# Optimization experiments

Hardware: AMD Instinct MI355X
Metric: run time of the kernel (lower is better)

## Reference

```python
import jax, jax.numpy as jnp
import numpy as np

B, C, H, W = 1, 320, 64, 64
HEADS, DHEAD = 8, 40
INNER = HEADS * DHEAD          # 320 == C (as in Stable Diffusion)
CTX_LEN, CTX_DIM = 77, 768
FF_INNER = 4 * INNER           # 1280
GROUPS, GN_EPS, LN_EPS = 32, 1e-6, 1e-5
SCALE = DHEAD ** -0.5


def setup_inputs() -> dict:
    key = jax.random.key(0)
    ks = jax.random.split(key, 16)
    def w(k, shape):
        return jax.random.normal(k, shape, jnp.float32) * 0.02
    return {
        'x': jax.random.normal(ks[0], (B, C, H, W), jnp.float32),
        'context': jax.random.normal(ks[1], (B, CTX_LEN, CTX_DIM), jnp.float32),
        'gn_scale': jnp.ones((C,), jnp.float32),
        'gn_bias': jnp.zeros((C,), jnp.float32),
        'w_proj_in': w(ks[2], (C, INNER)), 'b_proj_in': jnp.zeros((INNER,), jnp.float32),
        'ln1_s': jnp.ones((INNER,), jnp.float32), 'ln1_b': jnp.zeros((INNER,), jnp.float32),
        'wq1': w(ks[3], (INNER, INNER)), 'wk1': w(ks[4], (INNER, INNER)),
        'wv1': w(ks[5], (INNER, INNER)), 'wo1': w(ks[6], (INNER, INNER)),
        'bo1': jnp.zeros((INNER,), jnp.float32),
        'ln2_s': jnp.ones((INNER,), jnp.float32), 'ln2_b': jnp.zeros((INNER,), jnp.float32),
        'wq2': w(ks[7], (INNER, INNER)), 'wk2': w(ks[8], (CTX_DIM, INNER)),
        'wv2': w(ks[9], (CTX_DIM, INNER)), 'wo2': w(ks[10], (INNER, INNER)),
        'bo2': jnp.zeros((INNER,), jnp.float32),
        'ln3_s': jnp.ones((INNER,), jnp.float32), 'ln3_b': jnp.zeros((INNER,), jnp.float32),
        'w_ff1': w(ks[11], (INNER, 2 * FF_INNER)), 'b_ff1': jnp.zeros((2 * FF_INNER,), jnp.float32),
        'w_ff2': w(ks[12], (FF_INNER, INNER)), 'b_ff2': jnp.zeros((INNER,), jnp.float32),
        'w_proj_out': w(ks[13], (INNER, C)), 'b_proj_out': jnp.zeros((C,), jnp.float32),
    }


def _group_norm(x, scale, bias):
    b, c, h, w = x.shape
    xg = x.reshape(b, GROUPS, c // GROUPS, h, w)
    mu = xg.mean(axis=(2, 3, 4), keepdims=True)
    var = xg.var(axis=(2, 3, 4), keepdims=True)
    xg = (xg - mu) * jax.lax.rsqrt(var + GN_EPS)
    return xg.reshape(b, c, h, w) * scale[None, :, None, None] + bias[None, :, None, None]


def _layer_norm(x, s, b):
    mu = x.mean(-1, keepdims=True)
    var = x.var(-1, keepdims=True)
    return (x - mu) * jax.lax.rsqrt(var + LN_EPS) * s + b


def _attention(xq, ctx, wq, wk, wv, wo, bo):
    b, s, _ = xq.shape
    t = ctx.shape[1]
    q = (xq @ wq).reshape(b, s, HEADS, DHEAD)
    k = (ctx @ wk).reshape(b, t, HEADS, DHEAD)
    v = (ctx @ wv).reshape(b, t, HEADS, DHEAD)
    scores = jnp.einsum('bihd,bjhd->bhij', q, k) * SCALE  # [b,h,s,t]
    probs = jax.nn.softmax(scores, axis=-1)
    o = jnp.einsum('bhij,bjhd->bihd', probs, v).reshape(b, s, INNER)
    return o @ wo + bo


def _forward(x, context, gn_scale, gn_bias, w_proj_in, b_proj_in,
             ln1_s, ln1_b, wq1, wk1, wv1, wo1, bo1,
             ln2_s, ln2_b, wq2, wk2, wv2, wo2, bo2,
             ln3_s, ln3_b, w_ff1, b_ff1, w_ff2, b_ff2,
             w_proj_out, b_proj_out):
    x_in = x
    h_ = _group_norm(x, gn_scale, gn_bias)
    # 1x1 conv proj_in as channel matmul
    h_ = jnp.einsum('bchw,cd->bdhw', h_, w_proj_in) + b_proj_in[None, :, None, None]
    h_ = h_.transpose(0, 2, 3, 1).reshape(B, H * W, INNER)  # [b, s, d]
    # self-attention
    hn = _layer_norm(h_, ln1_s, ln1_b)
    h_ = _attention(hn, hn, wq1, wk1, wv1, wo1, bo1) + h_
    # cross-attention
    hn = _layer_norm(h_, ln2_s, ln2_b)
    h_ = _attention(hn, context, wq2, wk2, wv2, wo2, bo2) + h_
    # GEGLU feed-forward
    hn = _layer_norm(h_, ln3_s, ln3_b)
    y = hn @ w_ff1 + b_ff1
    a, g = jnp.split(y, 2, axis=-1)
    y = (a * jax.nn.gelu(g, approximate=False)) @ w_ff2 + b_ff2
    h_ = y + h_
    h_ = h_.reshape(B, H, W, INNER).transpose(0, 3, 1, 2)
    out = jnp.einsum('bchw,cd->bdhw', h_, w_proj_out) + b_proj_out[None, :, None, None]
    return out + x_in


def reference(x, context, gn_scale, gn_bias, w_proj_in, b_proj_in,
              ln1_s, ln1_b, wq1, wk1, wv1, wo1, bo1,
              ln2_s, ln2_b, wq2, wk2, wv2, wo2, bo2,
              ln3_s, ln3_b, w_ff1, b_ff1, w_ff2, b_ff2,
              w_proj_out, b_proj_out):
    return _forward(x, context, gn_scale, gn_bias, w_proj_in, b_proj_in,
                    ln1_s, ln1_b, wq1, wk1, wv1, wo1, bo1,
                    ln2_s, ln2_b, wq2, wk2, wv2, wo2, bo2,
                    ln3_s, ln3_b, w_ff1, b_ff1, w_ff2, b_ff2,
                    w_proj_out, b_proj_out)
```

## Files before the change

### kernel.cpp

```cpp
#include <hip/hip_runtime.h>
#include <hip/hip_bf16.h>
#include <math.h>

#define SCALE_L2E  0.22811011265722836f

typedef __attribute__((ext_vector_type(8))) short short8v;
typedef __attribute__((ext_vector_type(4))) float float4v;
typedef unsigned short u16;

__device__ __forceinline__ unsigned pack2(float a, float b) {
  float2 f; f.x = a; f.y = b;
  __hip_bfloat162 h = __float22bfloat162_rn(f);
  return *(unsigned*)&h;
}
__device__ __forceinline__ float bfu2f(u16 u) {
  return __uint_as_float(((unsigned)u) << 16);
}
__device__ __forceinline__ u16 f2bf(float x) {
  __hip_bfloat16 h = __float2bfloat16(x);
  return *(u16*)&h;
}

struct TDesc { const float* src; u16* dst; int K, N, off, tx; float sc; };
struct TPack { TDesc d[12]; };

__global__ __launch_bounds__(256) void prep_kernel(
    TPack p, int nT,
    const float* __restrict__ ctxsrc, u16* __restrict__ ctxdst,
    const float* __restrict__ x,
    float* __restrict__ psum, float* __restrict__ psq) {
  __shared__ float ls[32][33];
  int bt = blockIdx.x, t = threadIdx.x;
  if (bt < nT) {
    int ti = 0;
    #pragma unroll
    for (int i = 1; i < 12; i++) if (bt >= p.d[i].off) ti = i;
    TDesc dd = p.d[ti];
    int local = bt - dd.off;
    int n0 = (local % dd.tx) * 32, k0 = (local / dd.tx) * 32;
    #pragma unroll
    for (int i = 0; i < 4; i++) {
      int idx = t + i*256, r = idx >> 5, c = idx & 31;
      ls[r][c] = dd.src[(size_t)(k0 + r)*dd.N + n0 + c];
    }
    __syncthreads();
    #pragma unroll
    for (int i = 0; i < 2; i++) {
      int p2 = t + i*256, n = p2 >> 4, kp = (p2 & 15)*2;
      *(unsigned*)&dd.dst[(size_t)(n0 + n)*dd.K + k0 + kp] =
        pack2(ls[kp][n]*dd.sc, ls[kp+1][n]*dd.sc);
    }
  } else if (bt < nT + 58) {
    int idx = ((bt - nT)*256 + t)*4;
    if (idx < 59136) {
      float4 v = *(const float4*)&ctxsrc[idx];
      uint2 o; o.x = pack2(v.x, v.y); o.y = pack2(v.z, v.w);
      *(uint2*)&ctxdst[idx] = o;
    }
  } else {
    int pp = bt - nT - 58;
    int g = pp >> 3, part = pp & 7;
    size_t base = (size_t)g*40960 + (size_t)part*5120;
    float sum = 0.f, sq = 0.f;
    #pragma unroll
    for (int r = 0; r < 5; r++) {
      float4 v = *(const float4*)&x[base + (size_t)(t + r*256)*4];
      sum += v.x + v.y + v.z + v.w;
      sq  += v.x*v.x + v.y*v.y + v.z*v.z + v.w*v.w;
    }
    float* s1 = &ls[0][0];
    float* s2 = &ls[8][0] + 8;
    s1[t] = sum; s2[t] = sq; __syncthreads();
    for (int st = 128; st > 0; st >>= 1) {
      if (t < st) { s1[t] += s1[t+st]; s2[t] += s2[t+st]; }
      __syncthreads();
    }
    if (t == 0) { psum[pp] = s1[0]; psq[pp] = s2[0]; }
  }
}

__global__ __launch_bounds__(256) void gn_apply_t_kernel(
    const float* __restrict__ x, const float* __restrict__ psum,
    const float* __restrict__ psq, const float* __restrict__ gs,
    const float* __restrict__ gb, u16* __restrict__ gnT) {
  __shared__ float ts[64][65];
  __shared__ float scl[64], sft[64];
  int s0 = blockIdx.x * 64, c0 = blockIdx.y * 64;
  int t = threadIdx.x;
  if (t < 64) {
    int c = c0 + t, g = c / 10;
    float s = 0.f, q = 0.f;
    #pragma unroll
    for (int i = 0; i < 8; i++) { s += psum[g*8 + i]; q += psq[g*8 + i]; }
    float mu = s * (1.f/40960.f);
    float var = q * (1.f/40960.f) - mu*mu;
    float rs = rsqrtf(var + 1e-6f);
    float sc = rs * gs[c];
    scl[t] = sc;
    sft[t] = gb[c] - mu * sc;
  }
  int crow = t >> 2, sch = (t & 3) * 16;
  #pragma unroll
  for (int j = 0; j < 4; j++) {
    float4 v = *(const float4*)&x[(size_t)(c0 + crow)*4096 + s0 + sch + 4*j];
    ts[crow][sch + 4*j + 0] = v.x; ts[crow][sch + 4*j + 1] = v.y;
    ts[crow][sch + 4*j + 2] = v.z; ts[crow][sch + 4*j + 3] = v.w;
  }
  __syncthreads();
  int srow = t >> 2, cch = (t & 3) * 16;
  #pragma unroll
  for (int p = 0; p < 8; p++) {
    int cl = cch + 2*p;
    float f0 = ts[cl][srow] * scl[cl] + sft[cl];
    float f1 = ts[cl+1][srow] * scl[cl+1] + sft[cl+1];
    *(unsigned*)&gnT[(size_t)(s0 + srow)*320 + c0 + cl] = pack2(f0, f1);
  }
}

__global__ __launch_bounds__(64) void layernorm_kernel(
    const u16* __restrict__ X, const float* __restrict__ s,
    const float* __restrict__ b, u16* __restrict__ Y) {
  int row = blockIdx.x, t = threadIdx.x;
  const u16* xr = X + (size_t)row*320;
  float v[5], sum = 0.f, sq = 0.f;
  #pragma unroll
  for (int i = 0; i < 5; i++) { v[i] = bfu2f(xr[t + 64*i]); sum += v[i]; sq += v[i]*v[i]; }
  #pragma unroll
  for (int o = 32; o > 0; o >>= 1) { sum += __shfl_down(sum, o); sq += __shfl_down(sq, o); }
  sum = __shfl(sum, 0); sq = __shfl(sq, 0);
  float mu = sum * (1.f/320.f);
  float var = sq * (1.f/320.f) - mu*mu;
  float rs = rsqrtf(var + 1e-5f);
  u16* yr = Y + (size_t)row*320;
  #pragma unroll
  for (int i = 0; i < 5; i++) {
    int c = t + 64*i;
    yr[c] = f2bf((v[i]-mu)*rs*s[c] + b[c]);
  }
}

template<int MODE>
__global__ __launch_bounds__(256) void oneshot(
    const u16* __restrict__ A, const u16* __restrict__ BT,
    const float* __restrict__ bias, const u16* __restrict__ res,
    const float* __restrict__ xres, void* __restrict__ Cout,
    int K, int chunks) {
  __shared__ __align__(16) u16 As[64*328];
  __shared__ __align__(16) u16 Bs[32*328];
  const int t = threadIdx.x;
  const int lane = t & 63, w = t >> 6, l16 = lane & 15, g = lane >> 4;
  const int bm = blockIdx.x * 64, bn = blockIdx.y * 32;
  const int m0 = (w & 1) * 32, n0 = (w >> 1) * 16;
  float4v acc[2] = {};

  const u16* Ab = A + (size_t)(bm + (t>>2))*K + (t&3)*16;
  u16* Al = As + (t>>2)*328 + (t&3)*16;
  const u16* Bb = BT + (size_t)(bn + (t>>3))*K + (t&7)*16;
  u16* Bl = Bs + (t>>3)*328 + (t&7)*16;
  const bool b3 = (t & 7) < 4;

  for (int ch = 0; ch < chunks; ch++) {
    const int c0 = ch*320;
    __syncthreads();
    #pragma unroll
    for (int j = 0; j < 5; j++) {
      *(short8v*)(Al + 64*j)     = *(const short8v*)(Ab + c0 + 64*j);
      *(short8v*)(Al + 64*j + 8) = *(const short8v*)(Ab + c0 + 64*j + 8);
    }
    *(short8v*)Bl         = *(const short8v*)(Bb + c0);
    *(short8v*)(Bl + 8)   = *(const short8v*)(Bb + c0 + 8);
    *(short8v*)(Bl + 128) = *(const short8v*)(Bb + c0 + 128);
    *(short8v*)(Bl + 136) = *(const short8v*)(Bb + c0 + 136);
    if (b3) {
      *(short8v*)(Bl + 256) = *(const short8v*)(Bb + c0 + 256);
      *(short8v*)(Bl + 264) = *(const short8v*)(Bb + c0 + 264);
    }
    __syncthreads();
    #pragma unroll
    for (int ks = 0; ks < 10; ks++) {
      short8v bfv = *(const short8v*)&Bs[(n0 + l16)*328 + ks*32 + g*8];
      #pragma unroll
      for (int mt = 0; mt < 2; mt++) {
        short8v af = *(const short8v*)&As[(m0 + 16*mt + l16)*328 + ks*32 + g*8];
        acc[mt] = __builtin_amdgcn_mfma_f32_16x16x32_bf16(af, bfv, acc[mt], 0, 0, 0);
      }
    }
  }
  __syncthreads();
  float* Cs = (float*)As;
  #pragma unroll
  for (int mt = 0; mt < 2; mt++)
    #pragma unroll
    for (int r = 0; r < 4; r++)
      Cs[(m0 + 16*mt + 4*g + r)*36 + n0 + l16] = acc[mt][r];
  __syncthreads();

  if (MODE == 0) {
    u16* C = (u16*)Cout;
    #pragma unroll
    for (int i = 0; i < 4; i++) {
      int p = t + i*256;
      int mm = p >> 4, pp = (p & 15)*2;
      float f0 = Cs[mm*36 + pp], f1 = Cs[mm*36 + pp + 1];
      if (bias) { f0 += bias[bn + pp]; f1 += bias[bn + pp + 1]; }
      if (res) {
        unsigned u = *(const unsigned*)&res[(size_t)(bm + mm)*320 + bn + pp];
        f0 += bfu2f((u16)(u & 0xffffu));
        f1 += bfu2f((u16)(u >> 16));
      }
      *(unsigned*)&C[(size_t)(bm + mm)*320 + bn + pp] = pack2(f0, f1);
    }
  } else {
    float* C = (float*)Cout;
    int nloc = t >> 3, mch = (t & 7) * 8;
    float bb = bias[bn + nloc];
    #pragma unroll
    for (int j = 0; j < 2; j++) {
      int m4 = mch + j*4;
      float4 xv = *(const float4*)&xres[(size_t)(bn + nloc)*4096 + bm + m4];
      float4 ov;
      ov.x = Cs[(m4+0)*36 + nloc] + bb + xv.x;
      ov.y = Cs[(m4+1)*36 + nloc] + bb + xv.y;
      ov.z = Cs[(m4+2)*36 + nloc] + bb + xv.z;
      ov.w = Cs[(m4+3)*36 + nloc] + bb + xv.w;
      *(float4*)&C[(size_t)(bn + nloc)*4096 + bm + m4] = ov;
    }
  }
}

template<int MODE>
__global__ __launch_bounds__(256) void mgemm(
    const u16* __restrict__ A, const u16* __restrict__ BT,
    const float* __restrict__ bias, const u16* __restrict__ res,
    const float* __restrict__ xres, void* __restrict__ Cout,
    int M, int N, int K, int segStride) {
  __shared__ __align__(16) u16 smem[2*64*72];
  u16* As = smem;
  u16* Bs = smem + 64*72;
  const int t = threadIdx.x;
  const int lane = t & 63, w = t >> 6, l16 = lane & 15, g = lane >> 4;
  const int bm = blockIdx.x * 64, bn = blockIdx.y * 64;
  const int m0 = (w & 1) * 32, n0 = (w >> 1) * 32;
  float4v acc[2][2] = {};
  const int ar = t >> 2, ac = (t & 3) * 16;
  const bool aok = (bm + ar) < M;
  const u16* ga = &A[(size_t)(bm + ar)*K + ac];
  const u16* gb = &BT[(size_t)(bn + ar)*K + ac];

  short8v pa0 = {}, pa1 = {}, pb0, pb1;
  if (aok) { pa0 = *(const short8v*)ga; pa1 = *(const short8v*)(ga + 8); }
  pb0 = *(const short8v*)gb; pb1 = *(const short8v*)(gb + 8);

  for (int k0 = 0; k0 < K; k0 += 64) {
    __syncthreads();
    *(short8v*)&As[ar*72 + ac] = pa0;
    *(short8v*)&As[ar*72 + ac + 8] = pa1;
    *(short8v*)&Bs[ar*72 + ac] = pb0;
    *(short8v*)&Bs[ar*72 + ac + 8] = pb1;
    __syncthreads();
    if (k0 + 64 < K) {
      const u16* na = ga + k0 + 64;
      const u16* nb = gb + k0 + 64;
      if (aok) { pa0 = *(const short8v*)na; pa1 = *(const short8v*)(na + 8); }
      pb0 = *(const short8v*)nb; pb1 = *(const short8v*)(nb + 8);
    }
    #pragma unroll
    for (int ks = 0; ks < 2; ks++) {
      short8v af[2], bfv[2];
      #pragma unroll
      for (int mt = 0; mt < 2; mt++)
        af[mt] = *(const short8v*)&As[(m0 + 16*mt + l16)*72 + ks*32 + g*8];
      #pragma unroll
      for (int nt = 0; nt < 2; nt++)
        bfv[nt] = *(const short8v*)&Bs[(n0 + 16*nt + l16)*72 + ks*32 + g*8];
      #pragma unroll
      for (int mt = 0; mt < 2; mt++)
        #pragma unroll
        for (int nt = 0; nt < 2; nt++)
          acc[mt][nt] = __builtin_amdgcn_mfma_f32_16x16x32_bf16(af[mt], bfv[nt], acc[mt][nt], 0, 0, 0);
    }
  }
  __syncthreads();
  float* Cs = (float*)smem;
  #pragma unroll
  for (int mt = 0; mt < 2; mt++)
    #pragma unroll
    for (int nt = 0; nt < 2; nt++)
      #pragma unroll
      for (int r = 0; r < 4; r++)
        Cs[(m0 + 16*mt + 4*g + r)*68 + n0 + 16*nt + l16] = acc[mt][nt][r];
  __syncthreads();

  if (MODE == 1) {
    u16* C = (u16*)Cout + (size_t)(bn / 320) * segStride;
    int nb = bn % 320;
    #pragma unroll
    for (int i = 0; i < 8; i++) {
      int p = t + i*256;
      int mm = p >> 5, nn = (p & 31)*2;
      int gm = bm + mm;
      if (gm >= M) continue;
      *(unsigned*)&C[(size_t)gm*320 + nb + nn] = pack2(Cs[mm*68 + nn], Cs[mm*68 + nn + 1]);
    }
  } else if (MODE == 3) {
    if (bn < 640) {
      u16* C = (u16*)Cout + (size_t)(bn / 320) * segStride;
      int nb = bn % 320;
      #pragma unroll
      for (int i = 0; i < 8; i++) {
        int p = t + i*256;
        int mm = p >> 5, nn = (p & 31)*2;
        *(unsigned*)&C[(size_t)(bm + mm)*320 + nb + nn] = pack2(Cs[mm*68 + nn], Cs[mm*68 + nn + 1]);
      }
    } else {
      u16* vTp = (u16*)(void*)xres;
      int nloc = t >> 2, mch = (t & 3) * 16;
      int vd = bn - 640 + nloc;
      u16* dst = vTp + (size_t)vd*4096 + bm + mch;
      unsigned buf[8];
      #pragma unroll
      for (int jj = 0; jj < 8; jj++)
        buf[jj] = pack2(Cs[(mch + 2*jj)*68 + nloc], Cs[(mch + 2*jj + 1)*68 + nloc]);
      uint4 o0; o0.x = buf[0]; o0.y = buf[1]; o0.z = buf[2]; o0.w = buf[3];
      uint4 o1; o1.x = buf[4]; o1.y = buf[5]; o1.z = buf[6]; o1.w = buf[7];
      *(uint4*)dst = o0;
      *(uint4*)(dst + 8) = o1;
    }
  }
}

__global__ __launch_bounds__(256) void geglu_mfma(
    const u16* __restrict__ A, const u16* __restrict__ BT,
    const float* __restrict__ bias, u16* __restrict__ C) {
  __shared__ __align__(16) u16 smem[3*64*72];
  u16* As = smem;
  u16* Ba = smem + 64*72;
  u16* Bg = smem + 2*64*72;
  const int t = threadIdx.x;
  const int lane = t & 63, w = t >> 6, l16 = lane & 15, g = lane >> 4;
  const int bm = blockIdx.x * 64, bn = blockIdx.y * 64;
  const int m0 = (w & 1) * 32, n0 = (w >> 1) * 32;
  float4v aacc[2][2] = {}, gacc[2][2] = {};
  const int ar = t >> 2, ac = (t & 3) * 16;
  const u16* ga  = &A[(size_t)(bm + ar)*320 + ac];
  const u16* gba = &BT[(size_t)(bn + ar)*320 + ac];
  const u16* gbg = &BT[(size_t)(1280 + bn + ar)*320 + ac];

  short8v pa0 = *(const short8v*)ga,  pa1 = *(const short8v*)(ga + 8);
  short8v pb0 = *(const short8v*)gba, pb1 = *(const short8v*)(gba + 8);
  short8v pg0 = *(const short8v*)gbg, pg1 = *(const short8v*)(gbg + 8);

  for (int k0 = 0; k0 < 320; k0 += 64) {
    __syncthreads();
    *(short8v*)&As[ar*72 + ac] = pa0;
    *(short8v*)&As[ar*72 + ac + 8] = pa1;
    *(short8v*)&Ba[ar*72 + ac] = pb0;
    *(short8v*)&Ba[ar*72 + ac + 8] = pb1;
    *(short8v*)&Bg[ar*72 + ac] = pg0;
    *(short8v*)&Bg[ar*72 + ac + 8] = pg1;
    __syncthreads();
    if (k0 + 64 < 320) {
      pa0 = *(const short8v*)(ga + k0 + 64);  pa1 = *(const short8v*)(ga + k0 + 72);
      pb0 = *(const short8v*)(gba + k0 + 64); pb1 = *(const short8v*)(gba + k0 + 72);
      pg0 = *(const short8v*)(gbg + k0 + 64); pg1 = *(const short8v*)(gbg + k0 + 72);
    }
    #pragma unroll
    for (int ks = 0; ks < 2; ks++) {
      short8v af[2], bav[2], bgv[2];
      #pragma unroll
      for (int mt = 0; mt < 2; mt++)
        af[mt] = *(const short8v*)&As[(m0 + 16*mt + l16)*72 + ks*32 + g*8];
      #pragma unroll
      for (int nt = 0; nt < 2; nt++) {
        bav[nt] = *(const short8v*)&Ba[(n0 + 16*nt + l16)*72 + ks*32 + g*8];
        bgv[nt] = *(const short8v*)&Bg[(n0 + 16*nt + l16)*72 + ks*32 + g*8];
      }
      #pragma unroll
      for (int mt = 0; mt < 2; mt++)
        #pragma unroll
        for (int nt = 0; nt < 2; nt++) {
          aacc[mt][nt] = __builtin_amdgcn_mfma_f32_16x16x32_bf16(af[mt], bav[nt], aacc[mt][nt], 0, 0, 0);
          gacc[mt][nt] = __builtin_amdgcn_mfma_f32_16x16x32_bf16(af[mt], bgv[nt], gacc[mt][nt], 0, 0, 0);
        }
    }
  }
  __syncthreads();
  float* Cs = (float*)smem;
  #pragma unroll
  for (int nt = 0; nt < 2; nt++) {
    int col = n0 + 16*nt + l16;
    float ba = bias[bn + col];
    float bg2 = bias[1280 + bn + col];
    #pragma unroll
    for (int mt = 0; mt < 2; mt++)
      #pragma unroll
      for (int r = 0; r < 4; r++) {
        float a = aacc[mt][nt][r] + ba;
        float gv = gacc[mt][nt][r] + bg2;
        float gl = 0.5f * gv * (1.f + erff(gv * 0.70710678118654752f));
        Cs[(m0 + 16*mt + 4*g + r)*68 + col] = a * gl;
      }
  }
  __syncthreads();
  #pragma unroll
  for (int i = 0; i < 8; i++) {
    int p = t + i*256;
    int mm = p >> 5, nn = (p & 31)*2;
    *(unsigned*)&C[(size_t)(bm + mm)*1280 + bn + nn] = pack2(Cs[mm*68 + nn], Cs[mm*68 + nn + 1]);
  }
}

__global__ __launch_bounds__(512) void self_attn_part(
    const u16* __restrict__ Q, const u16* __restrict__ K,
    const u16* __restrict__ vT, u16* __restrict__ Opart,
    float* __restrict__ Lp) {
  const int h = blockIdx.y;
  const int q0 = blockIdx.x * 128;
  const int sp = blockIdx.z;
  const int tid = threadIdx.x;
  const int w = tid >> 6, lane = tid & 63;
  const int l16 = lane & 15, g = lane >> 4;

  __shared__ __align__(16) u16 Kls[64][72];
  __shared__ __align__(16) u16 Vt[48][72];
  __shared__ __align__(16) u16 PsT[8][16][72];

  for (int e = tid; e < 64*12; e += 512) {
    int r = e / 12, c = e % 12;
    *(unsigned*)&Kls[r][40 + 2*c] = 0u;
  }
  if (tid < 256) {
    int r = 40 + (tid >> 5), c = tid & 31;
    *(unsigned*)&Vt[r][2*c] = 0u;
  }

  short8v Qb[2];
  {
    const u16* qrow = Q + (size_t)(q0 + w*16 + l16)*320 + h*40;
    Qb[0] = *(const short8v*)(qrow + g*8);
    short8v z = {};
    Qb[1] = (g == 0) ? *(const short8v*)(qrow + 32) : z;
  }

  const u16* Kbase = K + (size_t)(sp*1024)*320 + h*40;
  const u16* Vbase = vT + (size_t)(h*40)*4096 + sp*1024;

  const int ksl = (tid < 320) ? tid : 0;
  const int keyK = ksl / 5, chK = ksl - keyK*5;
  const u16* gK = Kbase + (size_t)keyK*320 + chK*8;
  u16* lK = &Kls[keyK][chK*8];
  const int vsl = (tid >= 192) ? (tid - 192) : 0;
  const int dV = vsl >> 3, chV = vsl & 7;
  const u16* gV = Vbase + (size_t)dV*4096 + chV*8;
  u16* lV = &Vt[dV][chV*8];

  const bool doK = (tid < 320), doV = (tid >= 192);

  short8v rK = {}, rV = {};
  if (doK) rK = *(const short8v*)gK;
  if (doV) rV = *(const short8v*)gV;
  gK += 64*320; gV += 64;

  float l_i = 0.f;
  float4v Of[3] = {};

  for (int it = 0; it < 16; ++it) {
    __syncthreads();
    if (doK) *(short8v*)lK = rK;
    if (doV) *(short8v*)lV = rV;
    __syncthreads();
    if (it < 15) {
      if (doK) rK = *(const short8v*)gK;
      if (doV) rV = *(const short8v*)gV;
      gK += 64*320; gV += 64;
    }

    float4v Sf[4];
    #pragma unroll
    for (int mt = 0; mt < 4; mt++) {
      short8v ka0 = *(const short8v*)&Kls[mt*16 + l16][g*8];
      short8v ka1 = *(const short8v*)&Kls[mt*16 + l16][32 + g*8];
      float4v s = {};
      s = __builtin_amdgcn_mfma_f32_16x16x32_bf16(ka0, Qb[0], s, 0, 0, 0);
      s = __builtin_amdgcn_mfma_f32_16x16x32_bf16(ka1, Qb[1], s, 0, 0, 0);
      Sf[mt] = s;
    }

    float rsum = 0.f;
    #pragma unroll
    for (int mt = 0; mt < 4; mt++)
      #pragma unroll
      for (int r = 0; r < 4; r++) {
        float p = exp2f(Sf[mt][r]);
        Sf[mt][r] = p; rsum += p;
      }
    rsum += __shfl_xor(rsum, 16);
    rsum += __shfl_xor(rsum, 32);
    l_i += rsum;

    #pragma unroll
    for (int mt = 0; mt < 4; mt++) {
      uint2 pk;
      pk.x = pack2(Sf[mt][0], Sf[mt][1]);
      pk.y = pack2(Sf[mt][2], Sf[mt][3]);
      *(uint2*)&PsT[w][l16][mt*16 + 4*g] = pk;
    }
    asm volatile("s_waitcnt lgkmcnt(0)" ::: "memory");

    #pragma unroll
    for (int ks = 0; ks < 2; ks++) {
      short8v pb = *(const short8v*)&PsT[w][l16][ks*32 + g*8];
      #pragma unroll
      for (int mt = 0; mt < 3; mt++) {
        short8v va = *(const short8v*)&Vt[mt*16 + l16][ks*32 + g*8];
        Of[mt] = __builtin_amdgcn_mfma_f32_16x16x32_bf16(va, pb, Of[mt], 0, 0, 0);
      }
    }
  }

  const int q = q0 + w*16 + l16;
  u16* orow = Opart + (size_t)sp*4096*320 + (size_t)q*320 + h*40;
  #pragma unroll
  for (int mt = 0; mt < 3; mt++) {
    #pragma unroll
    for (int rp = 0; rp < 2; rp++) {
      int d = mt*16 + 4*g + rp*2;
      if (d < 40)
        *(unsigned*)&orow[d] = pack2(Of[mt][rp*2], Of[mt][rp*2+1]);
    }
  }
  if (g == 0)
    Lp[sp*32768 + q*8 + h] = l_i;
}

__global__ __launch_bounds__(256) void attn_merge(
    const u16* __restrict__ Opart, const float* __restrict__ Lp,
    u16* __restrict__ O) {
  int gid = blockIdx.x*256 + threadIdx.x;
  int dp = gid % 20;
  int qh = gid / 20;
  int q = qh >> 3, h = qh & 7;
  float ls = Lp[qh] + Lp[32768 + qh] + Lp[2*32768 + qh] + Lp[3*32768 + qh];
  size_t base = (size_t)q*320 + h*40 + dp*2;
  const size_t HBu = 4096u*320u;
  float r0 = 0.f, r1 = 0.f;
  #pragma unroll
  for (int sp = 0; sp < 4; sp++) {
    unsigned u = *(const unsigned*)&Opart[sp*HBu + base];
    r0 += bfu2f((u16)(u & 0xffffu));
    r1 += bfu2f((u16)(u >> 16));
  }
  float inv = 1.f / ls;
  *(unsigned*)&O[base] = pack2(r0*inv, r1*inv);
}

__global__ __launch_bounds__(256) void cross_attn_mfma(
    const u16* __restrict__ Q, const u16* __restrict__ Kc,
    const u16* __restrict__ Vc, u16* __restrict__ O) {
  const int h = blockIdx.y;
  const int q0 = blockIdx.x * 64;
  const int tid = threadIdx.x;
  const int w = tid >> 6, lane = tid & 63;
  const int l16 = lane & 15, g = lane >> 4;

  __shared__ __align__(16) u16 Kls[80][72];
  __shared__ __align__(16) u16 Vt[48][104];
  __shared__ __align__(16) u16 PsT[4][16][104];

  for (int e = tid; e < 80*12; e += 256) {
    int r = e / 12, c = e % 12;
    *(unsigned*)&Kls[r][40 + 2*c] = 0u;
  }
  for (int e = tid; e < 48*52; e += 256) {
    int r = e / 52, c = e % 52;
    *(unsigned*)&Vt[r][2*c] = 0u;
  }
  {
    int r = lane >> 2, c4 = (lane & 3)*4;
    uint2 z; z.x = 0u; z.y = 0u;
    *(uint2*)&PsT[w][r][80 + c4] = z;
  }

  short8v Qb[2];
  {
    const u16* qrow = Q + (size_t)(q0 + w*16 + l16)*320 + h*40;
    Qb[0] = *(const short8v*)(qrow + g*8);
    short8v z = {};
    Qb[1] = (g == 0) ? *(const short8v*)(qrow + 32) : z;
  }

  for (int e = tid; e < 1600; e += 256) {
    int key = e / 20, dp = e % 20;
    unsigned val = 0u;
    if (key < 77) val = *(const unsigned*)&Kc[(size_t)key*320 + h*40 + dp*2];
    *(unsigned*)&Kls[key][dp*2] = val;
  }
  __syncthreads();
  for (int e = tid; e < 1600; e += 256) {
    int kp = e / 40, d = e % 40;
    unsigned u0 = (kp*2     < 77) ? (unsigned)Vc[(size_t)(kp*2    )*320 + h*40 + d] : 0u;
    unsigned u1 = (kp*2 + 1 < 77) ? (unsigned)Vc[(size_t)(kp*2 + 1)*320 + h*40 + d] : 0u;
    *(unsigned*)&Vt[d][kp*2] = u0 | (u1 << 16);
  }
  __syncthreads();

  float4v Sf[5];
  #pragma unroll
  for (int mt = 0; mt < 5; mt++) {
    short8v ka0 = *(const short8v*)&Kls[mt*16 + l16][g*8];
    short8v ka1 = *(const short8v*)&Kls[mt*16 + l16][32 + g*8];
    float4v s = {};
    s = __builtin_amdgcn_mfma_f32_16x16x32_bf16(ka0, Qb[0], s, 0, 0, 0);
    s = __builtin_amdgcn_mfma_f32_16x16x32_bf16(ka1, Qb[1], s, 0, 0, 0);
    Sf[mt] = s;
  }

  float rsum = 0.f;
  #pragma unroll
  for (int mt = 0; mt < 5; mt++)
    #pragma unroll
    for (int r = 0; r < 4; r++) {
      int key = mt*16 + 4*g + r;
      float p = (key < 77) ? exp2f(Sf[mt][r]) : 0.f;
      Sf[mt][r] = p; rsum += p;
    }
  rsum += __shfl_xor(rsum, 16);
  rsum += __shfl_xor(rsum, 32);

  #pragma unroll
  for (int mt = 0; mt < 5; mt++) {
    uint2 pk;
    pk.x = pack2(Sf[mt][0], Sf[mt][1]);
    pk.y = pack2(Sf[mt][2], Sf[mt][3]);
    *(uint2*)&PsT[w][l16][mt*16 + 4*g] = pk;
  }
  __syncthreads();

  float4v Of[3] = {};
  #pragma unroll
  for (int ks = 0; ks < 3; ks++) {
    short8v pb = *(const short8v*)&PsT[w][l16][ks*32 + g*8];
    #pragma unroll
    for (int mt = 0; mt < 3; mt++) {
      short8v va = *(const short8v*)&Vt[mt*16 + l16][ks*32 + g*8];
      Of[mt] = __builtin_amdgcn_mfma_f32_16x16x32_bf16(va, pb, Of[mt], 0, 0, 0);
    }
  }

  float inv = 1.f / rsum;
  u16* orow = O + (size_t)(q0 + w*16 + l16)*320 + h*40;
  #pragma unroll
  for (int mt = 0; mt < 3; mt++) {
    #pragma unroll
    for (int rp = 0; rp < 2; rp++) {
      int d = mt*16 + 4*g + rp*2;
      if (d < 40)
        *(unsigned*)&orow[d] = pack2(Of[mt][rp*2] * inv, Of[mt][rp*2+1] * inv);
    }
  }
}

extern "C" void kernel_launch(void* const* d_in, const int* in_sizes, int n_in,
                              void* d_out, int out_size, void* d_ws, size_t ws_size,
                              hipStream_t stream) {
  const float* x        = (const float*)d_in[0];
  const float* ctx      = (const float*)d_in[1];
  const float* gn_s     = (const float*)d_in[2];
  const float* gn_b     = (const float*)d_in[3];
  const float* w_pin    = (const float*)d_in[4];
  const float* b_pin    = (const float*)d_in[5];
  const float* ln1_s    = (const float*)d_in[6];
  const float* ln1_b    = (const float*)d_in[7];
  const float* wq1      = (const float*)d_in[8];
  const float* wk1      = (const float*)d_in[9];
  const float* wv1      = (const float*)d_in[10];
  const float* wo1      = (const float*)d_in[11];
  const float* bo1      = (const float*)d_in[12];
  const float* ln2_s    = (const float*)d_in[13];
  const float* ln2_b    = (const float*)d_in[14];
  const float* wq2      = (const float*)d_in[15];
  const float* wk2      = (const float*)d_in[16];
  const float* wv2      = (const float*)d_in[17];
  const float* wo2      = (const float*)d_in[18];
  const float* bo2      = (const float*)d_in[19];
  const float* ln3_s    = (const float*)d_in[20];
  const float* ln3_b    = (const float*)d_in[21];
  const float* w_ff1    = (const float*)d_in[22];
  const float* b_ff1    = (const float*)d_in[23];
  const float* w_ff2    = (const float*)d_in[24];
  const float* b_ff2    = (const float*)d_in[25];
  const float* w_pout   = (const float*)d_in[26];
  const float* b_pout   = (const float*)d_in[27];
  float* out = (float*)d_out;

  u16* ws = (u16*)d_ws;
  const size_t HB = 4096u*320u;
  u16* h   = ws;
  u16* hn  = ws + HB;
  u16* q   = ws + 2*HB;
  u16* k   = ws + 3*HB;
  u16* vT  = ws + 4*HB;
  u16* ao  = ws + 5*HB;
  u16* gnT = k;
  u16* gg  = q;
  u16* wb  = ws + 6*HB;
  size_t o = 0;
  u16* ctxb   = wb + o; o += 59136;
  u16* wq1T   = wb + o; o += 102400;
  u16* wk1T   = wb + o; o += 102400;
  u16* wv1T   = wb + o; o += 102400;
  u16* wo1T   = wb + o; o += 102400;
  u16* wq2T   = wb + o; o += 102400;
  u16* wk2T   = wb + o; o += 245760;
  u16* wv2T   = wb + o; o += 245760;
  u16* wo2T   = wb + o; o += 102400;
  u16* wff1T  = wb + o; o += 819200;
  u16* wff2T  = wb + o; o += 409600;
  u16* wpoutT = wb + o; o += 102400;
  u16* wpinT  = wb + o; o += 102400;
  u16* kc     = wb + o; o += 24640;
  u16* vc     = wb + o; o += 24640;
  float* psum = (float*)(wb + o);
  float* psq  = psum + 256;
  u16* OpartB = (u16*)(psq + 256);
  float* Lpart = (float*)(OpartB + 4*HB);

  TPack tp;
  const float* srcs[12] = {wq1, wk1, wv1, wo1, wq2, wo2, w_pin, w_pout, wk2, wv2, w_ff1, w_ff2};
  u16* dsts[12]         = {wq1T, wk1T, wv1T, wo1T, wq2T, wo2T, wpinT, wpoutT, wk2T, wv2T, wff1T, wff2T};
  int Ks[12] = {320,320,320,320,320,320,320,320,768,768,320,1280};
  int Ns[12] = {320,320,320,320,320,320,320,320,320,320,2560,320};
  int off = 0;
  for (int i = 0; i < 12; i++) {
    tp.d[i].src = srcs[i]; tp.d[i].dst = dsts[i];
    tp.d[i].K = Ks[i]; tp.d[i].N = Ns[i];
    tp.d[i].off = off; tp.d[i].tx = Ns[i]/32;
    tp.d[i].sc = (i == 0 || i == 4) ? SCALE_L2E : 1.0f;
    off += (Ks[i]/32)*(Ns[i]/32);
  }

  dim3 blk(256), g64x10(64, 10), g64x5(64, 5);
  const u16* nres = nullptr;
  const float* nb = nullptr;

  hipLaunchKernelGGL(prep_kernel, dim3(off + 58 + 256), blk, 0, stream,
                     tp, off, ctx, ctxb, x, psum, psq);
  hipLaunchKernelGGL(gn_apply_t_kernel, g64x5, blk, 0, stream, x, psum, psq, gn_s, gn_b, gnT);
  hipLaunchKernelGGL((oneshot<0>), g64x10, blk, 0, stream, gnT, wpinT, b_pin, nres, nb, (void*)h, 320, 1);
  hipLaunchKernelGGL(layernorm_kernel, dim3(4096), dim3(64), 0, stream, h, ln1_s, ln1_b, hn);
  hipLaunchKernelGGL((mgemm<3>), dim3(64, 15), blk, 0, stream, hn, wq1T, nb, nres, (const float*)vT, (void*)q, 4096, 960, 320, (int)HB);
  hipLaunchKernelGGL(self_attn_part, dim3(32, 8, 4), dim3(512), 0, stream, q, k, vT, OpartB, Lpart);
  hipLaunchKernelGGL(attn_merge, dim3(2560), blk, 0, stream, OpartB, Lpart, ao);
  hipLaunchKernelGGL((oneshot<0>), g64x10, blk, 0, stream, ao, wo1T, bo1, h, nb, (void*)h, 320, 1);
  hipLaunchKernelGGL(layernorm_kernel, dim3(4096), dim3(64), 0, stream, h, ln2_s, ln2_b, hn);
  hipLaunchKernelGGL((oneshot<0>), g64x10, blk, 0, stream, hn, wq2T, nb, nres, nb, (void*)q, 320, 1);
  hipLaunchKernelGGL((mgemm<1>), dim3(2, 10), blk, 0, stream, ctxb, wk2T, nb, nres, nb, (void*)kc, 77, 640, 768, 24640);
  hipLaunchKernelGGL(cross_attn_mfma, dim3(64, 8), blk, 0, stream, q, kc, vc, ao);
  hipLaunchKernelGGL((oneshot<0>), g64x10, blk, 0, stream, ao, wo2T, bo2, h, nb, (void*)h, 320, 1);
  hipLaunchKernelGGL(layernorm_kernel, dim3(4096), dim3(64), 0, stream, h, ln3_s, ln3_b, hn);
  hipLaunchKernelGGL(geglu_mfma, dim3(64, 20), blk, 0, stream, hn, wff1T, b_ff1, gg);
  hipLaunchKernelGGL((oneshot<0>), g64x10, blk, 0, stream, gg, wff2T, b_ff2, h, nb, (void*)h, 1280, 4);
  hipLaunchKernelGGL((oneshot<2>), g64x10, blk, 0, stream, h, wpoutT, b_pout, nres, x, (void*)out, 320, 1);
}
```

Before: 292.9 us.

## Fuse cross-attn KV GEMM into GN kernel, one-shot QKV GEMM, MFMA row-sum

Merges the context K/V projection GEMM into the group-norm apply kernel as extra blocks, removing one launch and letting the two run concurrently. Replaces the K-looped QKV mgemm with a one-shot kernel that stages the full K=320 tile into LDS using 64x32 tiles (twice as many blocks). Computes the softmax denominator in self-attention through the MFMA by placing a row of ones in the padded V rows, which drops the per-iteration exp sum and shuffles. Adds larger LDS use per block and relies on padding columns of V for the sum.

```diff
diff --git a/kernel.cpp b/kernel.cpp
--- a/kernel.cpp
+++ b/kernel.cpp
@@ -79,41 +79,107 @@
   }
 }
 
-__global__ __launch_bounds__(256) void gn_apply_t_kernel(
+__global__ __launch_bounds__(256) void gn_kcvc(
     const float* __restrict__ x, const float* __restrict__ psum,
     const float* __restrict__ psq, const float* __restrict__ gs,
-    const float* __restrict__ gb, u16* __restrict__ gnT) {
-  __shared__ float ts[64][65];
+    const float* __restrict__ gb, u16* __restrict__ gnT,
+    const u16* __restrict__ ctxb, const u16* __restrict__ wk2T,
+    u16* __restrict__ kcvc) {
+  __shared__ __align__(16) u16 smem[2*64*72];
   __shared__ float scl[64], sft[64];
-  int s0 = blockIdx.x * 64, c0 = blockIdx.y * 64;
-  int t = threadIdx.x;
-  if (t < 64) {
-    int c = c0 + t, g = c / 10;
-    float s = 0.f, q = 0.f;
-    #pragma unroll
-    for (int i = 0; i < 8; i++) { s += psum[g*8 + i]; q += psq[g*8 + i]; }
-    float mu = s * (1.f/40960.f);
-    float var = q * (1.f/40960.f) - mu*mu;
-    float rs = rsqrtf(var + 1e-6f);
-    float sc = rs * gs[c];
-    scl[t] = sc;
-    sft[t] = gb[c] - mu * sc;
-  }
-  int crow = t >> 2, sch = (t & 3) * 16;
-  #pragma unroll
-  for (int j = 0; j < 4; j++) {
-    float4 v = *(const float4*)&x[(size_t)(c0 + crow)*4096 + s0 + sch + 4*j];
-    ts[crow][sch + 4*j + 0] = v.x; ts[crow][sch + 4*j + 1] = v.y;
-    ts[crow][sch + 4*j + 2] = v.z; ts[crow][sch + 4*j + 3] = v.w;
-  }
-  __syncthreads();
-  int srow = t >> 2, cch = (t & 3) * 16;
-  #pragma unroll
-  for (int p = 0; p < 8; p++) {
-    int cl = cch + 2*p;
-    float f0 = ts[cl][srow] * scl[cl] + sft[cl];
-    float f1 = ts[cl+1][srow] * scl[cl+1] + sft[cl+1];
-    *(unsigned*)&gnT[(size_t)(s0 + srow)*320 + c0 + cl] = pack2(f0, f1);
+  const int t = threadIdx.x;
+  if (blockIdx.x < 320) {
+    float* ts = (float*)smem;
+    int s0 = (blockIdx.x & 63) * 64, c0 = (blockIdx.x >> 6) * 64;
+    if (t < 64) {
+      int c = c0 + t, g = c / 10;
+      float s = 0.f, q = 0.f;
+      #pragma unroll
+      for (int i = 0; i < 8; i++) { s += psum[g*8 + i]; q += psq[g*8 + i]; }
+      float mu = s * (1.f/40960.f);
+      float var = q * (1.f/40960.f) - mu*mu;
+      float rs = rsqrtf(var + 1e-6f);
+      float sc = rs * gs[c];
+      scl[t] = sc;
+      sft[t] = gb[c] - mu * sc;
+    }
+    int crow = t >> 2, sch = (t & 3) * 16;
+    #pragma unroll
+    for (int j = 0; j < 4; j++) {
+      float4 v = *(const float4*)&x[(size_t)(c0 + crow)*4096 + s0 + sch + 4*j];
+      ts[crow*65 + sch + 4*j + 0] = v.x; ts[crow*65 + sch + 4*j + 1] = v.y;
+      ts[crow*65 + sch + 4*j + 2] = v.z; ts[crow*65 + sch + 4*j + 3] = v.w;
+    }
+    __syncthreads();
+    int srow = t >> 2, cch = (t & 3) * 16;
+    #pragma unroll
+    for (int p = 0; p < 8; p++) {
+      int cl = cch + 2*p;
+      float f0 = ts[cl*65 + srow] * scl[cl] + sft[cl];
+      float f1 = ts[(cl+1)*65 + srow] * scl[cl+1] + sft[cl+1];
+      *(unsigned*)&gnT[(size_t)(s0 + srow)*320 + c0 + cl] = pack2(f0, f1);
+    }
+  } else {
+    u16* As = smem;
+    u16* Bs = smem + 64*72;
+    const int lane = t & 63, w = t >> 6, l16 = lane & 15, g = lane >> 4;
+    int local = blockIdx.x - 320;
+    const int bm = (local & 1) * 64, bn = (local >> 1) * 64;
+    const int m0 = (w & 1) * 32, n0 = (w >> 1) * 32;
+    float4v acc[2][2] = {};
+    const int ar = t >> 2, ac = (t & 3) * 16;
+    const bool aok = (bm + ar) < 77;
+    const u16* ga = &ctxb[(size_t)(bm + ar)*768 + ac];
+    const u16* gbp = &wk2T[(size_t)(bn + ar)*768 + ac];
+    short8v pa0 = {}, pa1 = {}, pb0, pb1;
+    if (aok) { pa0 = *(const short8v*)ga; pa1 = *(const short8v*)(ga + 8); }
+    pb0 = *(const short8v*)gbp; pb1 = *(const short8v*)(gbp + 8);
+    for (int k0 = 0; k0 < 768; k0 += 64) {
+      __syncthreads();
+      *(short8v*)&As[ar*72 + ac] = pa0;
+      *(short8v*)&As[ar*72 + ac + 8] = pa1;
+      *(short8v*)&Bs[ar*72 + ac] = pb0;
+      *(short8v*)&Bs[ar*72 + ac + 8] = pb1;
+      __syncthreads();
+      if (k0 + 64 < 768) {
+        if (aok) { pa0 = *(const short8v*)(ga + k0 + 64); pa1 = *(const short8v*)(ga + k0 + 72); }
+        pb0 = *(const short8v*)(gbp + k0 + 64); pb1 = *(const short8v*)(gbp + k0 + 72);
+      }
+      #pragma unroll
+      for (int ks = 0; ks < 2; ks++) {
+        short8v af[2], bfv[2];
+        #pragma unroll
+        for (int mt = 0; mt < 2; mt++)
+          af[mt] = *(const short8v*)&As[(m0 + 16*mt + l16)*72 + ks*32 + g*8];
+        #pragma unroll
+        for (int nt = 0; nt < 2; nt++)
+          bfv[nt] = *(const short8v*)&Bs[(n0 + 16*nt + l16)*72 + ks*32 + g*8];
+        #pragma unroll
+        for (int mt = 0; mt < 2; mt++)
+          #pragma unroll
+          for (int nt = 0; nt < 2; nt++)
+            acc[mt][nt] = __builtin_amdgcn_mfma_f32_16x16x32_bf16(af[mt], bfv[nt], acc[mt][nt], 0, 0, 0);
+      }
+    }
+    __syncthreads();
+    float* Cs = (float*)smem;
+    #pragma unroll
+    for (int mt = 0; mt < 2; mt++)
+      #pragma unroll
+      for (int nt = 0; nt < 2; nt++)
+        #pragma unroll
+        for (int r = 0; r < 4; r++)
+          Cs[(m0 + 16*mt + 4*g + r)*68 + n0 + 16*nt + l16] = acc[mt][nt][r];
+    __syncthreads();
+    u16* C = kcvc + (size_t)(bn / 320) * 24640;
+    int nb = bn % 320;
+    #pragma unroll
+    for (int i = 0; i < 8; i++) {
+      int p = t + i*256;
+      int mm = p >> 5, nn = (p & 31)*2;
+      if (bm + mm >= 77) continue;
+      *(unsigned*)&C[(size_t)(bm + mm)*320 + nb + nn] = pack2(Cs[mm*68 + nn], Cs[mm*68 + nn + 1]);
+    }
   }
 }
 
@@ -228,104 +294,74 @@
   }
 }
 
-template<int MODE>
-__global__ __launch_bounds__(256) void mgemm(
+__global__ __launch_bounds__(256) void qkv_oneshot(
     const u16* __restrict__ A, const u16* __restrict__ BT,
-    const float* __restrict__ bias, const u16* __restrict__ res,
-    const float* __restrict__ xres, void* __restrict__ Cout,
-    int M, int N, int K, int segStride) {
-  __shared__ __align__(16) u16 smem[2*64*72];
-  u16* As = smem;
-  u16* Bs = smem + 64*72;
+    u16* __restrict__ qk, u16* __restrict__ vT, int segStride) {
+  __shared__ __align__(16) u16 As[64*328];
+  __shared__ __align__(16) u16 Bs[32*328];
   const int t = threadIdx.x;
   const int lane = t & 63, w = t >> 6, l16 = lane & 15, g = lane >> 4;
-  const int bm = blockIdx.x * 64, bn = blockIdx.y * 64;
-  const int m0 = (w & 1) * 32, n0 = (w >> 1) * 32;
-  float4v acc[2][2] = {};
-  const int ar = t >> 2, ac = (t & 3) * 16;
-  const bool aok = (bm + ar) < M;
-  const u16* ga = &A[(size_t)(bm + ar)*K + ac];
-  const u16* gb = &BT[(size_t)(bn + ar)*K + ac];
-
-  short8v pa0 = {}, pa1 = {}, pb0, pb1;
-  if (aok) { pa0 = *(const short8v*)ga; pa1 = *(const short8v*)(ga + 8); }
-  pb0 = *(const short8v*)gb; pb1 = *(const short8v*)(gb + 8);
-
-  for (int k0 = 0; k0 < K; k0 += 64) {
-    __syncthreads();
-    *(short8v*)&As[ar*72 + ac] = pa0;
-    *(short8v*)&As[ar*72 + ac + 8] = pa1;
-    *(short8v*)&Bs[ar*72 + ac] = pb0;
-    *(short8v*)&Bs[ar*72 + ac + 8] = pb1;
-    __syncthreads();
-    if (k0 + 64 < K) {
-      const u16* na = ga + k0 + 64;
-      const u16* nb = gb + k0 + 64;
-      if (aok) { pa0 = *(const short8v*)na; pa1 = *(const short8v*)(na + 8); }
-      pb0 = *(const short8v*)nb; pb1 = *(const short8v*)(nb + 8);
-    }
-    #pragma unroll
-    for (int ks = 0; ks < 2; ks++) {
-      short8v af[2], bfv[2];
-      #pragma unroll
-      for (int mt = 0; mt < 2; mt++)
-        af[mt] = *(const short8v*)&As[(m0 + 16*mt + l16)*72 + ks*32 + g*8];
-      #pragma unroll
-      for (int nt = 0; nt < 2; nt++)
-        bfv[nt] = *(const short8v*)&Bs[(n0 + 16*nt + l16)*72 + ks*32 + g*8];
-      #pragma unroll
-      for (int mt = 0; mt < 2; mt++)
-        #pragma unroll
-        for (int nt = 0; nt < 2; nt++)
-          acc[mt][nt] = __builtin_amdgcn_mfma_f32_16x16x32_bf16(af[mt], bfv[nt], acc[mt][nt], 0, 0, 0);
-    }
-  }
-  __syncthreads();
-  float* Cs = (float*)smem;
+  const int bm = blockIdx.x * 64, bn = blockIdx.y * 32;
+  const int m0 = (w & 1) * 32, n0 = (w >> 1) * 16;
+  float4v acc[2] = {};
+
+  const u16* Ab = A + (size_t)(bm + (t>>2))*320 + (t&3)*16;
+  u16* Al = As + (t>>2)*328 + (t&3)*16;
+  const u16* Bb = BT + (size_t)(bn + (t>>3))*320 + (t&7)*16;
+  u16* Bl = Bs + (t>>3)*328 + (t&7)*16;
+  const bool b3 = (t & 7) < 4;
+
+  #pragma unroll
+  for (int j = 0; j < 5; j++) {
+    *(short8v*)(Al + 64*j)     = *(const short8v*)(Ab + 64*j);
+    *(short8v*)(Al + 64*j + 8) = *(const short8v*)(Ab + 64*j + 8);
+  }
+  *(short8v*)Bl         = *(const short8v*)Bb;
+  *(short8v*)(Bl + 8)   = *(const short8v*)(Bb + 8);
+  *(short8v*)(Bl + 128) = *(const short8v*)(Bb + 128);
+  *(short8v*)(Bl + 136) = *(const short8v*)(Bb + 136);
+  if (b3) {
+    *(short8v*)(Bl + 256) = *(const short8v*)(Bb + 256);
+    *(short8v*)(Bl + 264) = *(const short8v*)(Bb + 264);
+  }
+  __syncthreads();
+  #pragma unroll
+  for (int ks = 0; ks < 10; ks++) {
+    short8v bfv = *(const short8v*)&Bs[(n0 + l16)*328 + ks*32 + g*8];
+    #pragma unroll
+    for (int mt = 0; mt < 2; mt++) {
+      short8v af = *(const short8v*)&As[(m0 + 16*mt + l16)*328 + ks*32 + g*8];
+      acc[mt] = __builtin_amdgcn_mfma_f32_16x16x32_bf16(af, bfv, acc[mt], 0, 0, 0);
+    }
+  }
+  __syncthreads();
+  float* Cs = (float*)As;
   #pragma unroll
   for (int mt = 0; mt < 2; mt++)
     #pragma unroll
-    for (int nt = 0; nt < 2; nt++)
-      #pragma unroll
-      for (int r = 0; r < 4; r++)
-        Cs[(m0 + 16*mt + 4*g + r)*68 + n0 + 16*nt + l16] = acc[mt][nt][r];
-  __syncthreads();
-
-  if (MODE == 1) {
-    u16* C = (u16*)Cout + (size_t)(bn / 320) * segStride;
+    for (int r = 0; r < 4; r++)
+      Cs[(m0 + 16*mt + 4*g + r)*36 + n0 + l16] = acc[mt][r];
+  __syncthreads();
+
+  if (bn < 640) {
+    u16* C = qk + (size_t)(bn / 320) * segStride;
     int nb = bn % 320;
     #pragma unroll
-    for (int i = 0; i < 8; i++) {
+    for (int i = 0; i < 4; i++) {
       int p = t + i*256;
-      int mm = p >> 5, nn = (p & 31)*2;
-      int gm = bm + mm;
-      if (gm >= M) continue;
-      *(unsigned*)&C[(size_t)gm*320 + nb + nn] = pack2(Cs[mm*68 + nn], Cs[mm*68 + nn + 1]);
-    }
-  } else if (MODE == 3) {
-    if (bn < 640) {
-      u16* C = (u16*)Cout + (size_t)(bn / 320) * segStride;
-      int nb = bn % 320;
-      #pragma unroll
-      for (int i = 0; i < 8; i++) {
-        int p = t + i*256;
-        int mm = p >> 5, nn = (p & 31)*2;
-        *(unsigned*)&C[(size_t)(bm + mm)*320 + nb + nn] = pack2(Cs[mm*68 + nn], Cs[mm*68 + nn + 1]);
-      }
-    } else {
-      u16* vTp = (u16*)(void*)xres;
-      int nloc = t >> 2, mch = (t & 3) * 16;
-      int vd = bn - 640 + nloc;
-      u16* dst = vTp + (size_t)vd*4096 + bm + mch;
-      unsigned buf[8];
-      #pragma unroll
-      for (int jj = 0; jj < 8; jj++)
-        buf[jj] = pack2(Cs[(mch + 2*jj)*68 + nloc], Cs[(mch + 2*jj + 1)*68 + nloc]);
-      uint4 o0; o0.x = buf[0]; o0.y = buf[1]; o0.z = buf[2]; o0.w = buf[3];
-      uint4 o1; o1.x = buf[4]; o1.y = buf[5]; o1.z = buf[6]; o1.w = buf[7];
-      *(uint4*)dst = o0;
-      *(uint4*)(dst + 8) = o1;
-    }
+      int mm = p >> 4, pp = (p & 15)*2;
+      *(unsigned*)&C[(size_t)(bm + mm)*320 + nb + pp] = pack2(Cs[mm*36 + pp], Cs[mm*36 + pp + 1]);
+    }
+  } else {
+    int nloc = t >> 3, mch = (t & 7) * 8;
+    int vd = bn - 640 + nloc;
+    u16* dst = vT + (size_t)vd*4096 + bm + mch;
+    uint4 o0;
+    o0.x = pack2(Cs[(mch+0)*36 + nloc], Cs[(mch+1)*36 + nloc]);
+    o0.y = pack2(Cs[(mch+2)*36 + nloc], Cs[(mch+3)*36 + nloc]);
+    o0.z = pack2(Cs[(mch+4)*36 + nloc], Cs[(mch+5)*36 + nloc]);
+    o0.w = pack2(Cs[(mch+6)*36 + nloc], Cs[(mch+7)*36 + nloc]);
+    *(uint4*)dst = o0;
   }
 }
 
@@ -431,7 +467,7 @@
   }
   if (tid < 256) {
     int r = 40 + (tid >> 5), c = tid & 31;
-    *(unsigned*)&Vt[r][2*c] = 0u;
+    *(unsigned*)&Vt[r][2*c] = (r == 40) ? 0x3F803F80u : 0u;
   }
 
   short8v Qb[2];
@@ -461,7 +497,6 @@
   if (doV) rV = *(const short8v*)gV;
   gK += 64*320; gV += 64;
 
-  float l_i = 0.f;
   float4v Of[3] = {};
 
   for (int it = 0; it < 16; ++it) {
@@ -486,17 +521,11 @@
       Sf[mt] = s;
     }
 
-    float rsum = 0.f;
     #pragma unroll
     for (int mt = 0; mt < 4; mt++)
       #pragma unroll
-      for (int r = 0; r < 4; r++) {
-        float p = exp2f(Sf[mt][r]);
-        Sf[mt][r] = p; rsum += p;
-      }
-    rsum += __shfl_xor(rsum, 16);
-    rsum += __shfl_xor(rsum, 32);
-    l_i += rsum;
+      for (int r = 0; r < 4; r++)
+        Sf[mt][r] = exp2f(Sf[mt][r]);
 
     #pragma unroll
     for (int mt = 0; mt < 4; mt++) {
@@ -529,8 +558,8 @@
         *(unsigned*)&orow[d] = pack2(Of[mt][rp*2], Of[mt][rp*2+1]);
     }
   }
-  if (g == 0)
-    Lp[sp*32768 + q*8 + h] = l_i;
+  if (g == 2)
+    Lp[sp*32768 + q*8 + h] = Of[2][0];
 }
 
 __global__ __launch_bounds__(256) void attn_merge(
@@ -739,22 +768,22 @@
     off += (Ks[i]/32)*(Ns[i]/32);
   }
 
-  dim3 blk(256), g64x10(64, 10), g64x5(64, 5);
+  dim3 blk(256), g64x10(64, 10);
   const u16* nres = nullptr;
   const float* nb = nullptr;
 
   hipLaunchKernelGGL(prep_kernel, dim3(off + 58 + 256), blk, 0, stream,
                      tp, off, ctx, ctxb, x, psum, psq);
-  hipLaunchKernelGGL(gn_apply_t_kernel, g64x5, blk, 0, stream, x, psum, psq, gn_s, gn_b, gnT);
+  hipLaunchKernelGGL(gn_kcvc, dim3(340), blk, 0, stream,
+                     x, psum, psq, gn_s, gn_b, gnT, ctxb, wk2T, kc);
   hipLaunchKernelGGL((oneshot<0>), g64x10, blk, 0, stream, gnT, wpinT, b_pin, nres, nb, (void*)h, 320, 1);
   hipLaunchKernelGGL(layernorm_kernel, dim3(4096), dim3(64), 0, stream, h, ln1_s, ln1_b, hn);
-  hipLaunchKernelGGL((mgemm<3>), dim3(64, 15), blk, 0, stream, hn, wq1T, nb, nres, (const float*)vT, (void*)q, 4096, 960, 320, (int)HB);
+  hipLaunchKernelGGL(qkv_oneshot, dim3(64, 30), blk, 0, stream, hn, wq1T, q, vT, (int)HB);
   hipLaunchKernelGGL(self_attn_part, dim3(32, 8, 4), dim3(512), 0, stream, q, k, vT, OpartB, Lpart);
   hipLaunchKernelGGL(attn_merge, dim3(2560), blk, 0, stream, OpartB, Lpart, ao);
   hipLaunchKernelGGL((oneshot<0>), g64x10, blk, 0, stream, ao, wo1T, bo1, h, nb, (void*)h, 320, 1);
   hipLaunchKernelGGL(layernorm_kernel, dim3(4096), dim3(64), 0, stream, h, ln2_s, ln2_b, hn);
   hipLaunchKernelGGL((oneshot<0>), g64x10, blk, 0, stream, hn, wq2T, nb, nres, nb, (void*)q, 320, 1);
-  hipLaunchKernelGGL((mgemm<1>), dim3(2, 10), blk, 0, stream, ctxb, wk2T, nb, nres, nb, (void*)kc, 77, 640, 768, 24640);
   hipLaunchKernelGGL(cross_attn_mfma, dim3(64, 8), blk, 0, stream, q, kc, vc, ao);
   hipLaunchKernelGGL((oneshot<0>), g64x10, blk, 0, stream, ao, wo2T, bo2, h, nb, (void*)h, 320, 1);
   hipLaunchKernelGGL(layernorm_kernel, dim3(4096), dim3(64), 0, stream, h, ln3_s, ln3_b, hn);
```

After: 289.7 us (median of 2 runs). No clear change (-1.1%).
